# Kernel tuning notes

Measured on AMD Instinct MI355X. Metric: run time of the kernel, lower is better.

## Reference

```python
import jax, jax.numpy as jnp
import numpy as np

B = 512
AUDIO_H, VIDEO_H, TEXT_H = 64, 64, 128
POST_DIM = 128
FUSION_DIM = (TEXT_H + 1) * (VIDEO_H + 1) * (AUDIO_H + 1)  # 129*65*65 = 545025


def setup_inputs() -> dict:
    key = jax.random.key(0)
    ks = jax.random.split(key, 9)
    s1 = 1.0 / np.sqrt(FUSION_DIM)
    s2 = 1.0 / np.sqrt(POST_DIM)
    return {
        "audio_h": jax.random.normal(ks[0], (B, AUDIO_H), jnp.float32),
        "video_h": jax.random.normal(ks[1], (B, VIDEO_H), jnp.float32),
        "text_h": jax.random.normal(ks[2], (B, TEXT_H), jnp.float32),
        "W1": jax.random.uniform(ks[3], (FUSION_DIM, POST_DIM), jnp.float32, -s1, s1),
        "b1": jax.random.uniform(ks[4], (POST_DIM,), jnp.float32, -s1, s1),
        "W2": jax.random.uniform(ks[5], (POST_DIM, POST_DIM), jnp.float32, -s2, s2),
        "b2": jax.random.uniform(ks[6], (POST_DIM,), jnp.float32, -s2, s2),
        "W3": jax.random.uniform(ks[7], (POST_DIM, 1), jnp.float32, -s2, s2),
        "b3": jax.random.uniform(ks[8], (1,), jnp.float32, -s2, s2),
    }


def reference(audio_h, video_h, text_h, W1, b1, W2, b2, W3, b3):
    b = audio_h.shape[0]
    ones = jnp.ones((b, 1), audio_h.dtype)
    a1 = jnp.concatenate([ones, audio_h], axis=1)  # [B, A+1]
    v1 = jnp.concatenate([ones, video_h], axis=1)  # [B, V+1]
    t1 = jnp.concatenate([ones, text_h], axis=1)   # [B, T+1]
    # trilinear outer product: [B, T+1, V+1, A+1]
    fusion = jnp.einsum('bi,bj,bk->bijk', t1, v1, a1)
    flat = fusion.reshape(b, -1)  # [B, FUSION_DIM]
    # post-fusion MLP (dropout probs = 0 -> identity at inference)
    y1 = jax.nn.relu(flat @ W1 + b1)
    y2 = jax.nn.relu(y1 @ W2 + b2)
    y3 = jax.nn.sigmoid(y2 @ W3 + b3)
    # affine map to [-3, 3]: output_range=6, output_shift=-3
    return y3 * 6.0 - 3.0
```

## Files before the change

kernel.cpp:

```cpp
#include <hip/hip_runtime.h>
#include <hip/hip_bf16.h>
#include <math.h>

#define POST 128
#define NI 129
#define NJK 4225
#define NTOT 16512
#define KBLKS 134
#define MBLKS 32
#define KHALF 67
#define PANEL_CLAMP 2163184u

typedef __attribute__((ext_vector_type(8))) short bf16x8;
typedef __attribute__((ext_vector_type(4))) float f32x4;
typedef __attribute__((ext_vector_type(4))) unsigned int u32x4;

__device__ __forceinline__ unsigned short f2bf(float f){
    unsigned u = __builtin_bit_cast(unsigned, f);
    unsigned r = (u + 0x7FFFu + ((u >> 16) & 1u)) >> 16;
    return (unsigned short)r;
}
__device__ __forceinline__ unsigned pack2(float a, float b){
    return (unsigned)f2bf(a) | ((unsigned)f2bf(b) << 16);
}
__device__ __forceinline__ unsigned cvtpk(float lo, float hi){
    unsigned r;
    asm("v_cvt_pk_bf16_f32 %0, %1, %2" : "=v"(r) : "v"(lo), "v"(hi));
    return r;
}

__device__ __forceinline__ void gload16(const void* g, void* l){
    __builtin_amdgcn_global_load_lds(
        (const __attribute__((address_space(1))) unsigned int*)g,
        (__attribute__((address_space(3))) unsigned int*)l, 16, 0, 0);
}

__global__ void build_af(const float* __restrict__ audio,
                         const float* __restrict__ video,
                         uint4* __restrict__ af)
{
    int gid = blockIdx.x * 256 + threadIdx.x;
    if (gid >= KBLKS * MBLKS * 64) return;
    int lane = gid & 63;
    int mblk = (gid >> 6) & 31;
    int kblk = gid >> 11;
    int m  = mblk * 16 + (lane & 15);
    int k0 = kblk * 32 + (lane >> 4) * 8;
    float vals[8];
#pragma unroll
    for (int j = 0; j < 8; ++j){
        int k = k0 + j;
        float p = 0.f;
        if (k < NJK){
            int jj = k / 65;
            int kk = k - jj * 65;
            float a = (kk == 0) ? 1.f : audio[m * 64 + kk - 1];
            float v = (jj == 0) ? 1.f : video[m * 64 + jj - 1];
            p = a * v;
        }
        vals[j] = p;
    }
    uint4 o;
    o.x = pack2(vals[0], vals[1]);
    o.y = pack2(vals[2], vals[3]);
    o.z = pack2(vals[4], vals[5]);
    o.w = pack2(vals[6], vals[7]);
    af[gid] = o;
}

__global__ __launch_bounds__(256, 4) void fusion_gemm(
    const float* __restrict__ W1,
    const uint4* __restrict__ af,
    float* __restrict__ Z0,
    float* __restrict__ Z1)
{
    __shared__ __align__(16) char lds[40960];

    int orig = blockIdx.x;
    int xcd  = orig & 7;
    int w    = xcd * 129 + (orig >> 3);
    int nt  = w >> 3;
    int sub = w & 7;
    int mt  = sub & 3;
    int kb  = sub >> 2;

    int t    = threadIdx.x;
    int lane = t & 63;
    int wv   = t >> 6;
    int wm   = wv >> 1, wn = wv & 1;

    f32x4 acc[4][4] = {};

    const char* wpanel = (const char*)(W1 + (size_t)nt * (NJK * 128));

    int n_c = t & 127;
    int kg  = t >> 7;

    int ks0 = kb * KHALF;

#define STAGE(ks_, pb_)                                                         \
    do {                                                                        \
        char* dst_ = lds + (pb_) * 16384;                                       \
        _Pragma("unroll")                                                       \
        for (int i_ = 0; i_ < 4; ++i_){                                         \
            int c_ = wv * 4 + i_;                                               \
            unsigned bo_ = (unsigned)(ks_) * 16384u                             \
                         + (unsigned)c_ * 1024u + (unsigned)lane * 16u;         \
            if (bo_ > PANEL_CLAMP) bo_ = PANEL_CLAMP;            \
            gload16(wpanel + bo_, dst_ + c_ * 1024);                            \
        }                                                                       \
    } while (0)

    STAGE(ks0, 0);

    for (int it = 0; it < KHALF; ++it){
        int ks = ks0 + it;
        int p  = it & 1;

        const uint4* abase = af + ((size_t)ks * 32 + mt * 8 + wm * 4) * 64 + lane;
        uint4 vA0 = abase[0];
        uint4 vA1 = abase[64];
        uint4 vA2 = abase[128];
        uint4 vA3 = abase[192];
        __builtin_amdgcn_sched_barrier(0);

        if (it + 1 < KHALF)
            STAGE(ks + 1, p ^ 1);
        __builtin_amdgcn_sched_barrier(0);

        if (it + 1 < KHALF){
            asm volatile("s_waitcnt vmcnt(8)" ::: "memory");
        } else {
            asm volatile("s_waitcnt vmcnt(4)" ::: "memory");
        }
        __builtin_amdgcn_sched_barrier(0);
        __builtin_amdgcn_s_barrier();

        {
            const char* rawp = lds + p * 16384;
            char* fragp      = lds + 32768;
            float v[16];
#pragma unroll
            for (int j = 0; j < 16; ++j)
                v[j] = *(const float*)(rawp + (kg * 16 + j) * 512 + n_c * 4);
            u32x4 u0, u1;
            u0.x = cvtpk(v[0],  v[1]);  u0.y = cvtpk(v[2],  v[3]);
            u0.z = cvtpk(v[4],  v[5]);  u0.w = cvtpk(v[6],  v[7]);
            u1.x = cvtpk(v[8],  v[9]);  u1.y = cvtpk(v[10], v[11]);
            u1.z = cvtpk(v[12], v[13]); u1.w = cvtpk(v[14], v[15]);
            int swz = ((n_c >> 1) & 3) << 4;
            *(u32x4*)(fragp + ((n_c * 64 + kg * 32     ) ^ swz)) = u0;
            *(u32x4*)(fragp + ((n_c * 64 + kg * 32 + 16) ^ swz)) = u1;
        }
        asm volatile("s_waitcnt lgkmcnt(0)" ::: "memory");
        __builtin_amdgcn_sched_barrier(0);
        __builtin_amdgcn_s_barrier();

        {
            const char* fragp = lds + 32768;
            bf16x8 b[4];
#pragma unroll
            for (int g = 0; g < 4; ++g){
                int n = wn * 64 + g * 16 + (lane & 15);
                int byte = (n * 64 + (lane >> 4) * 16) ^ (((n >> 1) & 3) << 4);
                b[g] = *(const bf16x8*)(fragp + byte);
            }
            bf16x8 a0 = __builtin_bit_cast(bf16x8, vA0);
            bf16x8 a1 = __builtin_bit_cast(bf16x8, vA1);
            bf16x8 a2 = __builtin_bit_cast(bf16x8, vA2);
            bf16x8 a3 = __builtin_bit_cast(bf16x8, vA3);
#pragma unroll
            for (int g = 0; g < 4; ++g){
                acc[0][g] = __builtin_amdgcn_mfma_f32_16x16x32_bf16(a0, b[g], acc[0][g], 0, 0, 0);
                acc[1][g] = __builtin_amdgcn_mfma_f32_16x16x32_bf16(a1, b[g], acc[1][g], 0, 0, 0);
                acc[2][g] = __builtin_amdgcn_mfma_f32_16x16x32_bf16(a2, b[g], acc[2][g], 0, 0, 0);
                acc[3][g] = __builtin_amdgcn_mfma_f32_16x16x32_bf16(a3, b[g], acc[3][g], 0, 0, 0);
            }
        }
    }

    float* Zp = kb ? Z1 : Z0;
    int row0 = mt * 128 + wm * 64 + (lane >> 4) * 4;
    int col0 = nt * 128 + wn * 64 + (lane & 15);
#pragma unroll
    for (int f = 0; f < 4; ++f)
#pragma unroll
        for (int g = 0; g < 4; ++g)
#pragma unroll
            for (int r = 0; r < 4; ++r)
                Zp[(size_t)(row0 + f * 16 + r) * NTOT + col0 + g * 16] = acc[f][g][r];
}

__global__ void tail_mlp(const float* __restrict__ Z0,
                         const float* __restrict__ Z1,
                         const float* __restrict__ text,
                         const float* __restrict__ b1,
                         const float* __restrict__ W2,
                         const float* __restrict__ b2,
                         const float* __restrict__ W3,
                         const float* __restrict__ b3,
                         float* __restrict__ out)
{
    int b   = blockIdx.x;
    int tid = threadIdx.x;
    __shared__ float t1s[NI];
    __shared__ float y1s[POST];
    __shared__ float red[2];

    t1s[tid + 1] = text[b * 128 + tid];
    if (tid == 0) t1s[0] = 1.f;
    __syncthreads();

    const float* z0 = Z0 + (size_t)b * NTOT;
    const float* z1 = Z1 + (size_t)b * NTOT;
    float acc = 0.f;
    for (int i = 0; i < NI; ++i)
        acc = fmaf(t1s[i], z0[i * 128 + tid] + z1[i * 128 + tid], acc);
    acc += b1[tid];
    float y1 = fmaxf(acc, 0.f);
    y1s[tid] = y1;
    __syncthreads();

    float a2 = b2[tid];
    for (int q = 0; q < 128; ++q)
        a2 = fmaf(y1s[q], W2[q * 128 + tid], a2);
    float y2 = fmaxf(a2, 0.f);

    float part = y2 * W3[tid];
#pragma unroll
    for (int off = 32; off > 0; off >>= 1)
        part += __shfl_down(part, off);
    if ((tid & 63) == 0) red[tid >> 6] = part;
    __syncthreads();
    if (tid == 0){
        float z = red[0] + red[1] + b3[0];
        out[b] = 6.f / (1.f + expf(-z)) - 3.f;
    }
}

extern "C" void kernel_launch(void* const* d_in, const int* in_sizes, int n_in,
                              void* d_out, int out_size, void* d_ws, size_t ws_size,
                              hipStream_t stream)
{
    const float* audio = (const float*)d_in[0];
    const float* video = (const float*)d_in[1];
    const float* text  = (const float*)d_in[2];
    const float* W1    = (const float*)d_in[3];
    const float* b1    = (const float*)d_in[4];
    const float* W2    = (const float*)d_in[5];
    const float* b2    = (const float*)d_in[6];
    const float* W3    = (const float*)d_in[7];
    const float* b3    = (const float*)d_in[8];
    float* out = (float*)d_out;

    char* ws = (char*)d_ws;
    uint4* af = (uint4*)ws;
    float* Z0 = (float*)(ws + (8u  << 20));
    float* Z1 = (float*)(ws + (48u << 20));

    int af_granules = KBLKS * MBLKS * 64;
    build_af<<<(af_granules + 255) / 256, 256, 0, stream>>>(audio, video, af);
    fusion_gemm<<<1032, 256, 0, stream>>>(W1, af, Z0, Z1);
    tail_mlp<<<512, 128, 0, stream>>>(Z0, Z1, text, b1, W2, b2, W3, b3, out);
}
```

Measured before the change: 182.3 us.

## Convert W1 fragments directly from swizzled fp32 LDS, dropping bf16 fragment stage

After: 188.2 us. 3.2% more time.

```diff
diff --git a/kernel.cpp b/kernel.cpp
--- a/kernel.cpp
+++ b/kernel.cpp
@@ -8,7 +8,7 @@
 #define NTOT 16512
 #define KBLKS 134
 #define MBLKS 32
-#define KHALF 67
+#define KSTEPS32 133
 #define PANEL_CLAMP 2163184u
 
 typedef __attribute__((ext_vector_type(8))) short bf16x8;
@@ -74,7 +74,7 @@
     float* __restrict__ Z0,
     float* __restrict__ Z1)
 {
-    __shared__ __align__(16) char lds[40960];
+    __shared__ __align__(16) char lds[32768];
 
     int orig = blockIdx.x;
     int xcd  = orig & 7;
@@ -84,6 +84,9 @@
     int mt  = sub & 3;
     int kb  = sub >> 2;
 
+    int ks0 = kb ? 67 : 0;
+    int ks1 = kb ? KSTEPS32 : 67;
+
     int t    = threadIdx.x;
     int lane = t & 63;
     int wv   = t >> 6;
@@ -93,42 +96,39 @@
 
     const char* wpanel = (const char*)(W1 + (size_t)nt * (NJK * 128));
 
-    int n_c = t & 127;
-    int kg  = t >> 7;
-
-    int ks0 = kb * KHALF;
-
 #define STAGE(ks_, pb_)                                                         \
     do {                                                                        \
-        char* dst_ = lds + (pb_) * 16384;                                       \
+        char* dstB_ = lds + (pb_) * 16384;                                      \
         _Pragma("unroll")                                                       \
         for (int i_ = 0; i_ < 4; ++i_){                                         \
-            int c_ = wv * 4 + i_;                                               \
+            int cb_ = wv * 4 + i_;                                              \
+            int k_  = 2 * cb_ + (lane >> 5);                                    \
+            int ngs_ = (lane & 31) ^ (((k_ >> 3) & 1) << 2);                    \
             unsigned bo_ = (unsigned)(ks_) * 16384u                             \
-                         + (unsigned)c_ * 1024u + (unsigned)lane * 16u;         \
+                         + (unsigned)k_ * 512u + (unsigned)ngs_ * 16u;          \
             if (bo_ > PANEL_CLAMP) bo_ = PANEL_CLAMP;            \
-            gload16(wpanel + bo_, dst_ + c_ * 1024);                            \
+            gload16(wpanel + bo_, dstB_ + cb_ * 1024);                          \
         }                                                                       \
     } while (0)
 
     STAGE(ks0, 0);
 
-    for (int it = 0; it < KHALF; ++it){
-        int ks = ks0 + it;
+    for (int ks = ks0; ks < ks1; ++ks){
+        int it = ks - ks0;
         int p  = it & 1;
 
-        const uint4* abase = af + ((size_t)ks * 32 + mt * 8 + wm * 4) * 64 + lane;
-        uint4 vA0 = abase[0];
-        uint4 vA1 = abase[64];
-        uint4 vA2 = abase[128];
-        uint4 vA3 = abase[192];
-        __builtin_amdgcn_sched_barrier(0);
-
-        if (it + 1 < KHALF)
+        const uint4* ab = af + ((size_t)ks * 32 + mt * 8 + wm * 4) * 64 + lane;
+        uint4 vA0 = ab[0];
+        uint4 vA1 = ab[64];
+        uint4 vA2 = ab[128];
+        uint4 vA3 = ab[192];
+        __builtin_amdgcn_sched_barrier(0);
+
+        if (ks + 1 < ks1)
             STAGE(ks + 1, p ^ 1);
         __builtin_amdgcn_sched_barrier(0);
 
-        if (it + 1 < KHALF){
+        if (ks + 1 < ks1){
             asm volatile("s_waitcnt vmcnt(8)" ::: "memory");
         } else {
             asm volatile("s_waitcnt vmcnt(4)" ::: "memory");
@@ -138,33 +138,27 @@
 
         {
             const char* rawp = lds + p * 16384;
-            char* fragp      = lds + 32768;
-            float v[16];
-#pragma unroll
-            for (int j = 0; j < 16; ++j)
-                v[j] = *(const float*)(rawp + (kg * 16 + j) * 512 + n_c * 4);
-            u32x4 u0, u1;
-            u0.x = cvtpk(v[0],  v[1]);  u0.y = cvtpk(v[2],  v[3]);
-            u0.z = cvtpk(v[4],  v[5]);  u0.w = cvtpk(v[6],  v[7]);
-            u1.x = cvtpk(v[8],  v[9]);  u1.y = cvtpk(v[10], v[11]);
-            u1.z = cvtpk(v[12], v[13]); u1.w = cvtpk(v[14], v[15]);
-            int swz = ((n_c >> 1) & 3) << 4;
-            *(u32x4*)(fragp + ((n_c * 64 + kg * 32     ) ^ swz)) = u0;
-            *(u32x4*)(fragp + ((n_c * 64 + kg * 32 + 16) ^ swz)) = u1;
-        }
-        asm volatile("s_waitcnt lgkmcnt(0)" ::: "memory");
-        __builtin_amdgcn_sched_barrier(0);
-        __builtin_amdgcn_s_barrier();
-
-        {
-            const char* fragp = lds + 32768;
+            int h  = lane >> 4;
+            int fx = (h & 1) << 2;
+
             bf16x8 b[4];
 #pragma unroll
             for (int g = 0; g < 4; ++g){
                 int n = wn * 64 + g * 16 + (lane & 15);
-                int byte = (n * 64 + (lane >> 4) * 16) ^ (((n >> 1) & 3) << 4);
-                b[g] = *(const bf16x8*)(fragp + byte);
+                const char* bp = rawp + (h * 8) * 512
+                               + (((n >> 2) ^ fx) * 16) + (n & 3) * 4;
+                float v[8];
+#pragma unroll
+                for (int j = 0; j < 8; ++j)
+                    v[j] = *(const float*)(bp + j * 512);
+                u32x4 ub;
+                ub.x = cvtpk(v[0], v[1]);
+                ub.y = cvtpk(v[2], v[3]);
+                ub.z = cvtpk(v[4], v[5]);
+                ub.w = cvtpk(v[6], v[7]);
+                b[g] = __builtin_bit_cast(bf16x8, ub);
             }
+
             bf16x8 a0 = __builtin_bit_cast(bf16x8, vA0);
             bf16x8 a1 = __builtin_bit_cast(bf16x8, vA1);
             bf16x8 a2 = __builtin_bit_cast(bf16x8, vA2);
@@ -177,6 +171,9 @@
                 acc[3][g] = __builtin_amdgcn_mfma_f32_16x16x32_bf16(a3, b[g], acc[3][g], 0, 0, 0);
             }
         }
+
+        __builtin_amdgcn_sched_barrier(0);
+        __builtin_amdgcn_s_barrier();
     }
 
     float* Zp = kb ? Z1 : Z0;
```
